# Performance work log

Measured on AMD Instinct MI355X. Metric: run time of the kernel, lower is better.

The kernel has to match this reference:

```python
import jax, jax.numpy as jnp
import numpy as np
from jax import lax

B, T, Tq, S, G, Hd, GW, V = 128, 512, 32, 64, 300, 256, 512, 159
Z = 7 * Hd + 2


def _gru_cell(x, h, Wih, Whh, bih, bhh):
    # torch.nn.GRUCell math (gate order r,z,n)
    gi = x @ Wih.T + bih
    gh = h @ Whh.T + bhh
    i_r, i_z, i_n = jnp.split(gi, 3, axis=-1)
    h_r, h_z, h_n = jnp.split(gh, 3, axis=-1)
    r = jax.nn.sigmoid(i_r + h_r)
    z = jax.nn.sigmoid(i_z + h_z)
    n = jnp.tanh(i_n + r * h_n)
    return (1.0 - z) * n + z * h


def _run_gru(x, Wih, Whh, bih, bhh):
    b = x.shape[0]
    h0 = jnp.zeros((b, Whh.shape[1]), x.dtype)
    def step(h, xt):
        h2 = _gru_cell(xt, h, Wih, Whh, bih, bhh)
        return h2, h2
    _, ys = lax.scan(step, h0, jnp.swapaxes(x, 0, 1))
    return jnp.swapaxes(ys, 0, 1)  # [B,T,H]


def _attention(C, Qv, Mv, zW, gW1, gb1, gW2, gb2):
    # Attention(C, Q, Mt_1) -> Attention_G(c, m=Q, q=Mt_1); vectorized over sentences.
    qb = Qv[:, None, :]   # question, 2nd arg 'm' in Attention_Z
    mb = Mv[:, None, :]   # memory,   3rd arg 'q' in Attention_Z
    cW = jnp.einsum('bsh,kh->bsk', C, zW)  # att_zW(c), no bias
    z = jnp.concatenate([
        C,
        jnp.broadcast_to(qb, C.shape),
        jnp.broadcast_to(mb, C.shape),
        C * mb,                       # c * q  (q = memory)
        C * qb,                       # c * m  (m = question)
        jnp.abs(C - mb),              # |c - q|
        jnp.abs(C - qb),              # |c - m|
        jnp.sum(cW * mb, -1, keepdims=True),  # diag(cW q^T)
        jnp.sum(cW * qb, -1, keepdims=True),  # diag(cW m^T)
    ], axis=-1)  # [B,S,7H+2]
    H1 = jnp.tanh(jnp.einsum('bsz,gz->bsg', z, gW1) + gb1)
    g = jax.nn.sigmoid(jnp.einsum('bsg,og->bso', H1, gW2) + gb2)
    return g[..., 0]  # [B,S]


def setup_inputs() -> dict:
    key = jax.random.key(0)
    ks = jax.random.split(key, 32)
    def p(k, shape):
        return jax.random.normal(k, shape, jnp.float32) * 0.05
    inp = {
        'input': jax.random.normal(ks[0], (B, T, G), jnp.float32),
        'Q': jax.random.normal(ks[1], (B, Tq, G), jnp.float32),
        'EOS_idx': jnp.sort(jax.random.randint(ks[2], (B, S), 0, T), axis=1),
        'q_seq_len': jax.random.randint(ks[3], (B,), 0, Tq),
        'm_depth': 3,
        'a_len': 1,
        # GRU_i
        'Wih_i': p(ks[4], (3 * Hd, G)), 'Whh_i': p(ks[5], (3 * Hd, Hd)),
        'bih_i': p(ks[6], (3 * Hd,)), 'bhh_i': p(ks[7], (3 * Hd,)),
        # GRU_q
        'Wih_q': p(ks[8], (3 * Hd, G)), 'Whh_q': p(ks[9], (3 * Hd, Hd)),
        'bih_q': p(ks[10], (3 * Hd,)), 'bhh_q': p(ks[11], (3 * Hd,)),
        # attention
        'zW': p(ks[12], (Hd, Hd)),
        'gW1': p(ks[13], (GW, Z)), 'gb1': p(ks[14], (GW,)),
        'gW2': p(ks[15], (1, GW)), 'gb2': p(ks[16], (1,)),
        # GRUcell_m
        'Wih_m': p(ks[17], (3 * Hd, Hd)), 'Whh_m': p(ks[18], (3 * Hd, Hd)),
        'bih_m': p(ks[19], (3 * Hd,)), 'bhh_m': p(ks[20], (3 * Hd,)),
        # answer module
        'Wa': p(ks[21], (V, Hd)),
        'Wih_a': p(ks[22], (3 * Hd, Hd + V)), 'Whh_a': p(ks[23], (3 * Hd, Hd)),
        'bih_a': p(ks[24], (3 * Hd,)), 'bhh_a': p(ks[25], (3 * Hd,)),
    }
    return inp


def reference(input, Q, EOS_idx, q_seq_len, m_depth, a_len,
              Wih_i, Whh_i, bih_i, bhh_i,
              Wih_q, Whh_q, bih_q, bhh_q,
              zW, gW1, gb1, gW2, gb2,
              Wih_m, Whh_m, bih_m, bhh_m,
              Wa, Wih_a, Whh_a, bih_a, bhh_a):
    b = input.shape[0]
    # InputModule2: GRU over words, gather hidden states at EOS positions -> facts
    out_i = _run_gru(input, Wih_i, Whh_i, bih_i, bhh_i)          # [B,T,H]
    facts = out_i[jnp.arange(b)[:, None], EOS_idx]               # [B,S,H]
    # QuestionModule2: last valid hidden state of question GRU
    out_q = _run_gru(Q, Wih_q, Whh_q, bih_q, bhh_q)              # [B,Tq,H]
    qidx = jnp.clip(q_seq_len - 1, 0, Q.shape[1] - 1)
    q = out_q[jnp.arange(b), qidx]                               # [B,H]
    # MemoryUpdate (mode='softmax')
    Mt = q
    atts = []
    for _ in range(m_depth):
        att = _attention(facts, q, Mt, zW, gW1, gb1, gW2, gb2)   # [B,S]
        atts.append(att[:, None, :])
        soft = jax.nn.softmax(att, axis=1)
        Htc = jnp.einsum('bsh,bs->bh', facts, soft)              # SoftmaxRep
        Mt = _gru_cell(Htc, Mt, Wih_m, Whh_m, bih_m, bhh_m)
    Attentions = jnp.concatenate(atts, axis=1)                   # [B,depth,S]
    # AnswerModule
    at = Mt
    yt = jax.nn.softmax(at @ Wa.T, axis=1)
    preds = []
    for _ in range(a_len):
        xt = jnp.concatenate([yt, q], axis=1)
        at = _gru_cell(xt, at, Wih_a, Whh_a, bih_a, bhh_a)
        yt = jax.nn.softmax(at @ Wa.T, axis=1)
        preds.append(yt)
    pred = jnp.concatenate(preds, axis=1)                        # [B, a_len*159]
    return pred
```

## Files before the change

### kernel.cpp

```cpp
#include <hip/hip_runtime.h>
#include <hip/hip_bf16.h>

#define B_   128
#define T_   512
#define TQ_  32
#define S_   64
#define G_   300
#define GP_  320
#define HD_  256
#define GW_  512
#define V_   159
#define Z_   1794
#define ZP_  1824
#define H3_  768

using bf16x8 = __attribute__((ext_vector_type(8))) short;
using bf16x4 = __attribute__((ext_vector_type(4))) short;
using f32x4  = __attribute__((ext_vector_type(4))) float;

#define OFF_WIHB_I 0u
#define OFF_WIHB_Q 491520u
#define OFF_GW1B   983040u
#define OFF_FACTS  2850816u
#define OFF_QVEC   11239424u
#define OFF_UQ     11370496u
#define OFF_UM     11501568u
#define OFF_MT     11632640u
#define OFF_HTC    11763712u
#define OFF_YT     12681216u
#define OFF_XT     12762624u
#define OFF_AT2    12975104u
#define OFF_ATT    13106176u
#define OFF_B2I    13139968u
#define OFF_B2Q    13143040u
#define OFF_ABF    16777216u
#define OFF_QBF    16777216u
#define OFF_GIQ    20971520u
#define OFF_Z      29360128u
#define OFF_WMXT   59768832u
#define OFF_WMHT   60555264u
#define OFF_WAXT   61341696u
#define OFF_WAHT   62616576u
#define OFF_GII    67108864u
#define OFF_H1     67108864u

#define WAIT_LGKM0() __builtin_amdgcn_s_waitcnt(0xC07F)

__device__ __forceinline__ unsigned short f2bf(float f) {
    unsigned int u = __float_as_uint(f);
    u += 0x7fffu + ((u >> 16) & 1u);
    return (unsigned short)(u >> 16);
}
__device__ __forceinline__ float bf2f(unsigned short s) {
    return __uint_as_float(((unsigned int)s) << 16);
}
__device__ __forceinline__ float rcpf(float x) { return __builtin_amdgcn_rcpf(x); }
__device__ __forceinline__ float sigm(float x) { return rcpf(1.f + __expf(-x)); }
__device__ __forceinline__ float tanh_fast(float x) {
    float e = __expf(-2.f * fabsf(x));
    float t = (1.f - e) * rcpf(1.f + e);
    return copysignf(t, x);
}

__global__ void conv_pad_kernel(const float* __restrict__ src, unsigned short* __restrict__ dst,
                                int M, int K, int Kp) {
    int i = blockIdx.x * 256 + threadIdx.x;
    if (i >= M * Kp) return;
    int r = i / Kp, c = i - r * Kp;
    dst[i] = (c < K) ? f2bf(src[(size_t)r * K + c]) : (unsigned short)0;
}

#define SEG_A  196608
#define SEG_C  318720
__global__ void prep_kernel(
    const float* __restrict__ Wih_m, float* __restrict__ WmxT,
    const float* __restrict__ Whh_m, float* __restrict__ WmhT,
    const float* __restrict__ Wih_a, float* __restrict__ WaxT,
    const float* __restrict__ Whh_a, float* __restrict__ WahT,
    const float* __restrict__ bih_i, const float* __restrict__ bhh_i, float* __restrict__ b2i,
    const float* __restrict__ bih_q, const float* __restrict__ bhh_q, float* __restrict__ b2q)
{
    int i = blockIdx.x * 256 + threadIdx.x;
    if (i < SEG_A) {
        int r = i / 256, k = i - r * 256;
        WmxT[(size_t)k * 768 + r] = Wih_m[i];
        WmhT[(size_t)k * 768 + r] = Whh_m[i];
        WahT[(size_t)k * 768 + r] = Whh_a[i];
        return;
    }
    i -= SEG_A;
    if (i < SEG_C) {
        int r = i / 415, k = i - r * 415;
        WaxT[(size_t)k * 768 + r] = Wih_a[i];
        return;
    }
    i -= SEG_C;
    if (i < 768) {
        b2i[i] = bih_i[i] + (i < 512 ? bhh_i[i] : 0.f);
        b2q[i] = bih_q[i] + (i < 512 ? bhh_q[i] : 0.f);
    }
}

__global__ __launch_bounds__(256) void gemm_bf16_kernel(
    const unsigned short* __restrict__ A, const unsigned short* __restrict__ W,
    const float* __restrict__ bias, void* __restrict__ Cout,
    int M, int N, int Kp, int act, int out_bf16, int mode, int logT)
{
    __shared__ unsigned short As[64][40];
    __shared__ unsigned short Bs[64][40];
    int tid  = threadIdx.x;
    int wv   = tid >> 6, lane = tid & 63;
    int l15  = lane & 15, q = lane >> 4;
    int n0   = blockIdx.x * 64, m0 = blockIdx.y * 64;
    int r    = tid >> 2, p4 = tid & 3;

    const f32x4 zero4 = {0.f, 0.f, 0.f, 0.f};
    f32x4 acc[4] = {zero4, zero4, zero4, zero4};

    for (int k0 = 0; k0 < Kp; k0 += 32) {
        *(int4*)&As[r][p4 * 8] = *(const int4*)&A[(size_t)(m0 + r) * Kp + k0 + p4 * 8];
        *(int4*)&Bs[r][p4 * 8] = *(const int4*)&W[(size_t)(n0 + r) * Kp + k0 + p4 * 8];
        __syncthreads();
        bf16x8 af = *(const bf16x8*)&As[16 * wv + l15][q * 8];
#pragma unroll
        for (int nt = 0; nt < 4; nt++) {
            bf16x8 bf = *(const bf16x8*)&Bs[16 * nt + l15][q * 8];
            acc[nt] = __builtin_amdgcn_mfma_f32_16x16x32_bf16(af, bf, acc[nt], 0, 0, 0);
        }
        __syncthreads();
    }
    int rb = q * 4;
#pragma unroll
    for (int nt = 0; nt < 4; nt++) {
        int cgate = n0 + 16 * nt + l15;
        float bv = bias ? bias[cgate] : 0.f;
#pragma unroll
        for (int i = 0; i < 4; i++) {
            int row = m0 + 16 * wv + rb + i;
            float v = acc[nt][i] + bv;
            if (act == 1) v = tanh_fast(v);
            if (mode == 1) {
                int Tl = 1 << logT;
                int b = row >> logT, t = row & (Tl - 1);
                int cc = b >> 4, l = b & 15;
                int type = cgate >> 8, h = cgate & 255;
                int wvd = h >> 5, off = h & 31;
                int ttd = off >> 4, qd = (off >> 2) & 3, id = off & 3;
                int tidd = wvd * 64 + qd * 16 + l;
                size_t addr = ((size_t)(cc * Tl + t) * 512 + tidd) * 24 + type * 8 + ttd * 4 + id;
                ((unsigned short*)Cout)[addr] = f2bf(v);
            } else if (out_bf16) {
                ((unsigned short*)Cout)[(size_t)row * N + cgate] = f2bf(v);
            } else {
                ((float*)Cout)[(size_t)row * N + cgate] = v;
            }
        }
    }
}

__global__ __launch_bounds__(512, 2) void gru_rec_kernel(
    const float* __restrict__ Whh0, const float* __restrict__ bhh0,
    const unsigned short* __restrict__ gi0, int T0, const int* __restrict__ g0, int GL0,
    float* __restrict__ dst0,
    const float* __restrict__ Whh1, const float* __restrict__ bhh1,
    const unsigned short* __restrict__ gi1, int T1, const int* __restrict__ g1, int GL1,
    float* __restrict__ dst1)
{
    __shared__ unsigned short hfr[2][8][4][16][8];
    __shared__ int glist[16 * 64];
    __shared__ int gptr[16], gr0s[2][16], gr1s[2][16];
    extern __shared__ unsigned short wnL[];

    int cb  = blockIdx.x;
    int tid = threadIdx.x;
    int wv  = tid >> 6, lane = tid & 63;
    int l15 = lane & 15, q = lane >> 4;

    const float* Whh; const float* bhh; const unsigned short* gi;
    const int* gidx; float* gdst; int T, GL, isq, c;
    if (cb < 8) { Whh = Whh0; bhh = bhh0; gi = gi0; T = T0; gidx = g0; GL = GL0; isq = 0; gdst = dst0; c = cb; }
    else        { Whh = Whh1; bhh = bhh1; gi = gi1; T = T1; gidx = g1; GL = GL1; isq = 1; gdst = dst1; c = cb - 8; }

    bf16x8 wf[5][8];
#pragma unroll
    for (int mt = 0; mt < 5; mt++) {
        int type = (mt < 4) ? (mt >> 1) : 2;
        int tt   = (mt < 4) ? (mt & 1) : 0;
        int g = type * 256 + 32 * wv + 16 * tt + l15;
#pragma unroll
        for (int ks = 0; ks < 8; ks++) {
            float4 w0 = *(const float4*)&Whh[(size_t)g * 256 + ks * 32 + q * 8];
            float4 w1 = *(const float4*)&Whh[(size_t)g * 256 + ks * 32 + q * 8 + 4];
            bf16x8 v;
            v[0] = (short)f2bf(w0.x); v[1] = (short)f2bf(w0.y);
            v[2] = (short)f2bf(w0.z); v[3] = (short)f2bf(w0.w);
            v[4] = (short)f2bf(w1.x); v[5] = (short)f2bf(w1.y);
            v[6] = (short)f2bf(w1.z); v[7] = (short)f2bf(w1.w);
            wf[mt][ks] = v;
        }
    }
    {
        int g = 512 + 32 * wv + 16 + l15;
#pragma unroll
        for (int ks = 0; ks < 8; ks++) {
            float4 w0 = *(const float4*)&Whh[(size_t)g * 256 + ks * 32 + q * 8];
            float4 w1 = *(const float4*)&Whh[(size_t)g * 256 + ks * 32 + q * 8 + 4];
            bf16x8 v;
            v[0] = (short)f2bf(w0.x); v[1] = (short)f2bf(w0.y);
            v[2] = (short)f2bf(w0.z); v[3] = (short)f2bf(w0.w);
            v[4] = (short)f2bf(w1.x); v[5] = (short)f2bf(w1.y);
            v[6] = (short)f2bf(w1.z); v[7] = (short)f2bf(w1.w);
            *(bf16x8*)&wnL[((wv * 8 + ks) * 64 + lane) * 8] = v;
        }
    }
    float bn[2][4];
#pragma unroll
    for (int tt = 0; tt < 2; tt++)
#pragma unroll
        for (int i = 0; i < 4; i++)
            bn[tt][i] = bhh[512 + 32 * wv + 16 * tt + 4 * q + i];

    for (int i2 = tid; i2 < 2048; i2 += 512) ((int*)hfr)[i2] = 0;
    for (int i2 = tid; i2 < 16 * GL; i2 += 512) {
        int b = i2 / GL, s = i2 - b * GL;
        int raw = gidx[(c * 16 + b) * GL + s];
        if (isq) { raw -= 1; if (raw < 0) raw = 0; if (raw > T - 1) raw = T - 1; }
        glist[b * 64 + s] = raw;
    }
    __syncthreads();
    if (tid < 16) {
        int p = 0;
        while (p < GL && glist[tid * 64 + p] == 0) p++;
        gr0s[0][tid] = 0; gr1s[0][tid] = p; gptr[tid] = p;
    }
    __syncthreads();

    float hprev[2][4] = {{0.f, 0.f, 0.f, 0.f}, {0.f, 0.f, 0.f, 0.f}};
    const unsigned short* gib = gi + (size_t)c * T * 12288;
    bf16x8 xa, xb, xc;
    {
        const unsigned short* pv = gib + (size_t)tid * 24;
        xa = *(const bf16x8*)pv;
        xb = *(const bf16x8*)(pv + 8);
        xc = *(const bf16x8*)(pv + 16);
    }

    const f32x4 zero4 = {0.f, 0.f, 0.f, 0.f};
    for (int t = 0; t < T; t++) {
        int cur = t & 1, nxt = cur ^ 1;
        if (tid < 16) {
            int tt1 = t + 1;
            int p = gptr[tid], pp = p;
            while (p < GL && glist[tid * 64 + p] == tt1) p++;
            gr0s[nxt][tid] = pp; gr1s[nxt][tid] = p; gptr[tid] = p;
        }
        f32x4 acc[6];
        acc[0] = zero4; acc[1] = zero4; acc[2] = zero4; acc[3] = zero4;
        {
            f32x4 b4 = {bn[0][0], bn[0][1], bn[0][2], bn[0][3]}; acc[4] = b4;
            f32x4 b5 = {bn[1][0], bn[1][1], bn[1][2], bn[1][3]}; acc[5] = b5;
        }
#pragma unroll
        for (int ks = 0; ks < 8; ks++) {
            bf16x8 hb = *(const bf16x8*)&hfr[cur][ks][q][l15][0];
            acc[0] = __builtin_amdgcn_mfma_f32_16x16x32_bf16(wf[0][ks], hb, acc[0], 0, 0, 0);
            acc[1] = __builtin_amdgcn_mfma_f32_16x16x32_bf16(wf[1][ks], hb, acc[1], 0, 0, 0);
            acc[2] = __builtin_amdgcn_mfma_f32_16x16x32_bf16(wf[2][ks], hb, acc[2], 0, 0, 0);
            acc[3] = __builtin_amdgcn_mfma_f32_16x16x32_bf16(wf[3][ks], hb, acc[3], 0, 0, 0);
            acc[4] = __builtin_amdgcn_mfma_f32_16x16x32_bf16(wf[4][ks], hb, acc[4], 0, 0, 0);
            bf16x8 w5 = *(const bf16x8*)&wnL[((wv * 8 + ks) * 64 + lane) * 8];
            acc[5] = __builtin_amdgcn_mfma_f32_16x16x32_bf16(w5, hb, acc[5], 0, 0, 0);
        }
        float h2a[2][4];
#pragma unroll
        for (int tt = 0; tt < 2; tt++) {
#pragma unroll
            for (int i = 0; i < 4; i++) {
                float r = sigm(bf2f((unsigned short)xa[tt * 4 + i]) + acc[tt][i]);
                float z = sigm(bf2f((unsigned short)xb[tt * 4 + i]) + acc[2 + tt][i]);
                float n = tanh_fast(bf2f((unsigned short)xc[tt * 4 + i]) + r * acc[4 + tt][i]);
                float h2 = (1.f - z) * n + z * hprev[tt][i];
                hprev[tt][i] = h2;
                h2a[tt][i] = h2;
            }
            bf16x4 hb;
#pragma unroll
            for (int i = 0; i < 4; i++) hb[i] = (short)f2bf(h2a[tt][i]);
            int qp = 2 * tt + (q >> 1), jb = 4 * (q & 1);
            *(bf16x4*)&hfr[nxt][wv][qp][l15][jb] = hb;
        }
        {
            int p0 = gr0s[cur][l15], p1 = gr1s[cur][l15];
            for (int s = p0; s < p1; s++) {
                float* dp = &gdst[((size_t)(c * 16 + l15) * GL + s) * 256 + 32 * wv + 4 * q];
                float4 o0 = {h2a[0][0], h2a[0][1], h2a[0][2], h2a[0][3]};
                float4 o1 = {h2a[1][0], h2a[1][1], h2a[1][2], h2a[1][3]};
                *(float4*)dp        = o0;
                *(float4*)(dp + 16) = o1;
            }
        }
        {
            int tn = (t + 1 < T) ? (t + 1) : (T - 1);
            const unsigned short* pv = gib + ((size_t)tn * 512 + tid) * 24;
            xa = *(const bf16x8*)pv;
            xb = *(const bf16x8*)(pv + 8);
            xc = *(const bf16x8*)(pv + 16);
        }
        __builtin_amdgcn_sched_barrier(0);
        WAIT_LGKM0();
        __builtin_amdgcn_s_barrier();
        __builtin_amdgcn_sched_barrier(0);
    }
}

__global__ __launch_bounds__(256) void uvec_kernel(const float* __restrict__ zW,
                                                   const float* __restrict__ v,
                                                   float* __restrict__ u,
                                                   float* __restrict__ vcopy) {
    int b = blockIdx.x, h = threadIdx.x;
    float a = 0.f;
    for (int k = 0; k < 256; k++) a += zW[k * 256 + h] * v[b * 256 + k];
    u[b * 256 + h] = a;
    if (vcopy) vcopy[b * 256 + h] = v[b * 256 + h];
}

__global__ __launch_bounds__(256) void build_z_kernel(
    const float* __restrict__ facts, const float* __restrict__ qv, const float* __restrict__ Mt,
    const float* __restrict__ u_m, const float* __restrict__ u_q, unsigned short* __restrict__ z)
{
    __shared__ float rm[4], rq[4], szm, szq;
    int bs = blockIdx.x;
    int b  = bs >> 6;
    int j  = threadIdx.x;
    float C  = facts[(size_t)bs * 256 + j];
    float m  = Mt[b * 256 + j];
    float qq = qv[b * 256 + j];
    float dm = C * u_m[b * 256 + j];
    float dq = C * u_q[b * 256 + j];
    for (int o = 32; o; o >>= 1) { dm += __shfl_down(dm, o); dq += __shfl_down(dq, o); }
    int wvi = j >> 6;
    if ((j & 63) == 0) { rm[wvi] = dm; rq[wvi] = dq; }
    __syncthreads();
    if (j == 0) { szm = rm[0] + rm[1] + rm[2] + rm[3]; szq = rq[0] + rq[1] + rq[2] + rq[3]; }
    __syncthreads();
    size_t zr = (size_t)bs * ZP_;
    z[zr + j]        = f2bf(C);
    z[zr + 256 + j]  = f2bf(qq);
    z[zr + 512 + j]  = f2bf(m);
    z[zr + 768 + j]  = f2bf(C * m);
    z[zr + 1024 + j] = f2bf(C * qq);
    z[zr + 1280 + j] = f2bf(fabsf(C - m));
    z[zr + 1536 + j] = f2bf(fabsf(C - qq));
    if (j == 0) { z[zr + 1792] = f2bf(szm); z[zr + 1793] = f2bf(szq); }
    if (j < ZP_ - Z_) z[zr + Z_ + j] = 0;
}

__global__ __launch_bounds__(256) void g_reduce_kernel(const float* __restrict__ H1,
                                                       const float* __restrict__ gW2,
                                                       const float* __restrict__ gb2,
                                                       float* __restrict__ att) {
    __shared__ float r[4];
    int row = blockIdx.x, tid = threadIdx.x;
    float a = H1[(size_t)row * 512 + tid] * gW2[tid]
            + H1[(size_t)row * 512 + 256 + tid] * gW2[256 + tid];
    for (int o = 32; o; o >>= 1) a += __shfl_down(a, o);
    if ((tid & 63) == 0) r[tid >> 6] = a;
    __syncthreads();
    if (tid == 0) att[row] = sigm(r[0] + r[1] + r[2] + r[3] + gb2[0]);
}

__global__ __launch_bounds__(256) void soft_htc_kernel(const float* __restrict__ att,
                                                       const float* __restrict__ facts,
                                                       float* __restrict__ Htc) {
    __shared__ float p[64];
    int b = blockIdx.x, tid = threadIdx.x;
    if (tid < 64) p[tid] = att[b * 64 + tid];
    __syncthreads();
    if (tid == 0) {
        float mx = -1e30f;
        for (int s = 0; s < 64; s++) mx = fmaxf(mx, p[s]);
        float sm = 0.f;
        for (int s = 0; s < 64; s++) { float e = __expf(p[s] - mx); p[s] = e; sm += e; }
        float inv = rcpf(sm);
        for (int s = 0; s < 64; s++) p[s] *= inv;
    }
    __syncthreads();
    float a = 0.f;
    for (int s = 0; s < 64; s++) a += facts[((size_t)b * 64 + s) * 256 + tid] * p[s];
    Htc[b * 256 + tid] = a;
}

__global__ __launch_bounds__(256) void cell_kernel(
    const float* __restrict__ x, int Kx, const float* __restrict__ WxT, const float* __restrict__ bx,
    const float* __restrict__ h, const float* __restrict__ WhT, const float* __restrict__ bh,
    float* __restrict__ hnew)
{
    __shared__ float xs[416], hs[256];
    int b = blockIdx.x, j = threadIdx.x;
    for (int i = j; i < Kx; i += 256) xs[i] = x[(size_t)b * Kx + i];
    hs[j] = h[b * 256 + j];
    __syncthreads();
    float ar = bx[j], az = bx[256 + j], an = bx[512 + j];
    for (int k = 0; k < Kx; k++) {
        float xv = xs[k];
        const float* wr = &WxT[(size_t)k * 768];
        ar += xv * wr[j]; az += xv * wr[256 + j]; an += xv * wr[512 + j];
    }
    float hr = bh[j], hz = bh[256 + j], hn = bh[512 + j];
    for (int k = 0; k < 256; k++) {
        float hv = hs[k];
        const float* wr = &WhT[(size_t)k * 768];
        hr += hv * wr[j]; hz += hv * wr[256 + j]; hn += hv * wr[512 + j];
    }
    float r = sigm(ar + hr);
    float z = sigm(az + hz);
    float n = tanh_fast(an + r * hn);
    hnew[b * 256 + j] = (1.f - z) * n + z * hs[j];
}

__global__ __launch_bounds__(256) void matvec_softmax_kernel(const float* __restrict__ src,
                                                             const float* __restrict__ Wa,
                                                             float* __restrict__ dst) {
    __shared__ float sc[V_];
    int b = blockIdx.x, tid = threadIdx.x;
    if (tid < V_) {
        float a = 0.f;
        for (int k = 0; k < 256; k++) a += src[b * 256 + k] * Wa[tid * 256 + k];
        sc[tid] = a;
    }
    __syncthreads();
    if (tid == 0) {
        float mx = -1e30f;
        for (int v = 0; v < V_; v++) mx = fmaxf(mx, sc[v]);
        float sm = 0.f;
        for (int v = 0; v < V_; v++) { float e = __expf(sc[v] - mx); sc[v] = e; sm += e; }
        float inv = rcpf(sm);
        for (int v = 0; v < V_; v++) sc[v] *= inv;
    }
    __syncthreads();
    if (tid < V_) dst[b * V_ + tid] = sc[tid];
}

__global__ void concat_xt_kernel(const float* __restrict__ yt, const float* __restrict__ qv,
                                 float* __restrict__ xt) {
    int i = blockIdx.x * 256 + threadIdx.x;
    if (i >= 128 * 415) return;
    int b = i / 415, j = i - b * 415;
    xt[i] = (j < V_) ? yt[b * V_ + j] : qv[b * 256 + (j - V_)];
}

extern "C" void kernel_launch(void* const* d_in, const int* in_sizes, int n_in,
                              void* d_out, int out_size, void* d_ws, size_t ws_size,
                              hipStream_t stream) {
    (void)in_sizes; (void)n_in; (void)out_size; (void)ws_size;
    const float* input = (const float*)d_in[0];
    const float* Qin   = (const float*)d_in[1];
    const int*   EOS   = (const int*)d_in[2];
    const int*   qsl   = (const int*)d_in[3];
    const float* Wih_i = (const float*)d_in[6];
    const float* Whh_i = (const float*)d_in[7];
    const float* bih_i = (const float*)d_in[8];
    const float* bhh_i = (const float*)d_in[9];
    const float* Wih_q = (const float*)d_in[10];
    const float* Whh_q = (const float*)d_in[11];
    const float* bih_q = (const float*)d_in[12];
    const float* bhh_q = (const float*)d_in[13];
    const float* zW    = (const float*)d_in[14];
    const float* gW1   = (const float*)d_in[15];
    const float* gb1   = (const float*)d_in[16];
    const float* gW2   = (const float*)d_in[17];
    const float* gb2   = (const float*)d_in[18];
    const float* Wih_m = (const float*)d_in[19];
    const float* Whh_m = (const float*)d_in[20];
    const float* bih_m = (const float*)d_in[21];
    const float* bhh_m = (const float*)d_in[22];
    const float* Wa    = (const float*)d_in[23];
    const float* Wih_a = (const float*)d_in[24];
    const float* Whh_a = (const float*)d_in[25];
    const float* bih_a = (const float*)d_in[26];
    const float* bhh_a = (const float*)d_in[27];

    char* ws = (char*)d_ws;
    unsigned short* Wihb_i = (unsigned short*)(ws + OFF_WIHB_I);
    unsigned short* Wihb_q = (unsigned short*)(ws + OFF_WIHB_Q);
    unsigned short* gW1b   = (unsigned short*)(ws + OFF_GW1B);
    float* facts = (float*)(ws + OFF_FACTS);
    float* qvec  = (float*)(ws + OFF_QVEC);
    float* u_q   = (float*)(ws + OFF_UQ);
    float* u_m   = (float*)(ws + OFF_UM);
    float* Mt    = (float*)(ws + OFF_MT);
    float* Htc   = (float*)(ws + OFF_HTC);
    float* yt    = (float*)(ws + OFF_YT);
    float* xt    = (float*)(ws + OFF_XT);
    float* at2   = (float*)(ws + OFF_AT2);
    float* att   = (float*)(ws + OFF_ATT);
    float* b2i   = (float*)(ws + OFF_B2I);
    float* b2q   = (float*)(ws + OFF_B2Q);
    float* WmxT  = (float*)(ws + OFF_WMXT);
    float* WmhT  = (float*)(ws + OFF_WMHT);
    float* WaxT  = (float*)(ws + OFF_WAXT);
    float* WahT  = (float*)(ws + OFF_WAHT);
    unsigned short* Abf  = (unsigned short*)(ws + OFF_ABF);
    unsigned short* Qbf  = (unsigned short*)(ws + OFF_QBF);
    unsigned short* gi_q = (unsigned short*)(ws + OFF_GIQ);
    unsigned short* zbf  = (unsigned short*)(ws + OFF_Z);
    unsigned short* gi_i = (unsigned short*)(ws + OFF_GII);
    float* H1 = (float*)(ws + OFF_H1);

    hipFuncSetAttribute((const void*)gru_rec_kernel,
                        hipFuncAttributeMaxDynamicSharedMemorySize, 65536);

    conv_pad_kernel<<<(65536 * GP_ + 255) / 256, 256, 0, stream>>>(input, Abf, 65536, G_, GP_);
    conv_pad_kernel<<<(H3_ * GP_ + 255) / 256, 256, 0, stream>>>(Wih_i, Wihb_i, H3_, G_, GP_);
    conv_pad_kernel<<<(H3_ * GP_ + 255) / 256, 256, 0, stream>>>(Wih_q, Wihb_q, H3_, G_, GP_);
    conv_pad_kernel<<<(GW_ * ZP_ + 255) / 256, 256, 0, stream>>>(gW1, gW1b, GW_, Z_, ZP_);
    prep_kernel<<<(SEG_A + SEG_C + 768 + 255) / 256, 256, 0, stream>>>(
        Wih_m, WmxT, Whh_m, WmhT, Wih_a, WaxT, Whh_a, WahT,
        bih_i, bhh_i, b2i, bih_q, bhh_q, b2q);
    gemm_bf16_kernel<<<dim3(12, 1024), 256, 0, stream>>>(Abf, Wihb_i, b2i, gi_i, 65536, H3_, GP_, 0, 1, 1, 9);
    conv_pad_kernel<<<(4096 * GP_ + 255) / 256, 256, 0, stream>>>(Qin, Qbf, 4096, G_, GP_);
    gemm_bf16_kernel<<<dim3(12, 64), 256, 0, stream>>>(Qbf, Wihb_q, b2q, gi_q, 4096, H3_, GP_, 0, 1, 1, 5);
    gru_rec_kernel<<<16, 512, 65536, stream>>>(Whh_i, bhh_i, gi_i, T_, EOS, S_, facts,
                                               Whh_q, bhh_q, gi_q, TQ_, qsl, 1, qvec);
    uvec_kernel<<<128, 256, 0, stream>>>(zW, qvec, u_q, Mt);
    for (int ep = 0; ep < 3; ep++) {
        uvec_kernel<<<128, 256, 0, stream>>>(zW, Mt, u_m, nullptr);
        build_z_kernel<<<8192, 256, 0, stream>>>(facts, qvec, Mt, u_m, u_q, zbf);
        gemm_bf16_kernel<<<dim3(8, 128), 256, 0, stream>>>(zbf, gW1b, gb1, H1, 8192, GW_, ZP_, 1, 0, 0, 0);
        g_reduce_kernel<<<8192, 256, 0, stream>>>(H1, gW2, gb2, att);
        soft_htc_kernel<<<128, 256, 0, stream>>>(att, facts, Htc);
        cell_kernel<<<128, 256, 0, stream>>>(Htc, 256, WmxT, bih_m, Mt, WmhT, bhh_m, Mt);
    }
    matvec_softmax_kernel<<<128, 256, 0, stream>>>(Mt, Wa, yt);
    concat_xt_kernel<<<(128 * 415 + 255) / 256, 256, 0, stream>>>(yt, qvec, xt);
    cell_kernel<<<128, 256, 0, stream>>>(xt, 415, WaxT, bih_a, Mt, WahT, bhh_a, at2);
    matvec_softmax_kernel<<<128, 256, 0, stream>>>(at2, Wa, (float*)d_out);
}
```

Measured before the change: 1.802 ms.

## Fuse episode tail, answer and prep kernels; prefetch GRU inputs two steps ahead

```diff
diff --git a/kernel.cpp b/kernel.cpp
--- a/kernel.cpp
+++ b/kernel.cpp
@@ -26,15 +26,10 @@
 #define OFF_UQ     11370496u
 #define OFF_UM     11501568u
 #define OFF_MT     11632640u
-#define OFF_HTC    11763712u
-#define OFF_YT     12681216u
-#define OFF_XT     12762624u
-#define OFF_AT2    12975104u
-#define OFF_ATT    13106176u
 #define OFF_B2I    13139968u
 #define OFF_B2Q    13143040u
+#define OFF_QBF    13500416u
 #define OFF_ABF    16777216u
-#define OFF_QBF    16777216u
 #define OFF_GIQ    20971520u
 #define OFF_Z      29360128u
 #define OFF_WMXT   59768832u
@@ -70,34 +65,62 @@
     dst[i] = (c < K) ? f2bf(src[(size_t)r * K + c]) : (unsigned short)0;
 }
 
-#define SEG_A  196608
-#define SEG_C  318720
+#define S1_ 196608
+#define S2_ 318720
+#define S3_ 768
+#define S4_ 245760
+#define S5_ 933888
+#define S6_ 1310720
+#define PREP_TOT (S1_ + S2_ + S3_ + S4_ + S5_ + S6_)
 __global__ void prep_kernel(
     const float* __restrict__ Wih_m, float* __restrict__ WmxT,
     const float* __restrict__ Whh_m, float* __restrict__ WmhT,
     const float* __restrict__ Wih_a, float* __restrict__ WaxT,
     const float* __restrict__ Whh_a, float* __restrict__ WahT,
     const float* __restrict__ bih_i, const float* __restrict__ bhh_i, float* __restrict__ b2i,
-    const float* __restrict__ bih_q, const float* __restrict__ bhh_q, float* __restrict__ b2q)
+    const float* __restrict__ bih_q, const float* __restrict__ bhh_q, float* __restrict__ b2q,
+    const float* __restrict__ Wih_i, unsigned short* __restrict__ Wihb_i,
+    const float* __restrict__ Wih_q, unsigned short* __restrict__ Wihb_q,
+    const float* __restrict__ gW1,   unsigned short* __restrict__ gW1b,
+    const float* __restrict__ Qin,   unsigned short* __restrict__ Qbf)
 {
     int i = blockIdx.x * 256 + threadIdx.x;
-    if (i < SEG_A) {
+    if (i < S1_) {
         int r = i / 256, k = i - r * 256;
         WmxT[(size_t)k * 768 + r] = Wih_m[i];
         WmhT[(size_t)k * 768 + r] = Whh_m[i];
         WahT[(size_t)k * 768 + r] = Whh_a[i];
         return;
     }
-    i -= SEG_A;
-    if (i < SEG_C) {
+    i -= S1_;
+    if (i < S2_) {
         int r = i / 415, k = i - r * 415;
         WaxT[(size_t)k * 768 + r] = Wih_a[i];
         return;
     }
-    i -= SEG_C;
-    if (i < 768) {
+    i -= S2_;
+    if (i < S3_) {
         b2i[i] = bih_i[i] + (i < 512 ? bhh_i[i] : 0.f);
         b2q[i] = bih_q[i] + (i < 512 ? bhh_q[i] : 0.f);
+        return;
+    }
+    i -= S3_;
+    if (i < S4_) {
+        int r = i / GP_, c = i - r * GP_;
+        Wihb_i[i] = (c < G_) ? f2bf(Wih_i[(size_t)r * G_ + c]) : (unsigned short)0;
+        Wihb_q[i] = (c < G_) ? f2bf(Wih_q[(size_t)r * G_ + c]) : (unsigned short)0;
+        return;
+    }
+    i -= S4_;
+    if (i < S5_) {
+        int r = i / ZP_, c = i - r * ZP_;
+        gW1b[i] = (c < Z_) ? f2bf(gW1[(size_t)r * Z_ + c]) : (unsigned short)0;
+        return;
+    }
+    i -= S5_;
+    if (i < S6_) {
+        int r = i / GP_, c = i - r * GP_;
+        Qbf[i] = (c < G_) ? f2bf(Qin[(size_t)r * G_ + c]) : (unsigned short)0;
     }
 }
 
@@ -237,16 +260,17 @@
 
     float hprev[2][4] = {{0.f, 0.f, 0.f, 0.f}, {0.f, 0.f, 0.f, 0.f}};
     const unsigned short* gib = gi + (size_t)c * T * 12288;
-    bf16x8 xa, xb, xc;
+    const f32x4 zero4 = {0.f, 0.f, 0.f, 0.f};
+
+    bf16x8 xa0, xb0, xc0, xa1, xb1, xc1;
     {
         const unsigned short* pv = gib + (size_t)tid * 24;
-        xa = *(const bf16x8*)pv;
-        xb = *(const bf16x8*)(pv + 8);
-        xc = *(const bf16x8*)(pv + 16);
-    }
-
-    const f32x4 zero4 = {0.f, 0.f, 0.f, 0.f};
-    for (int t = 0; t < T; t++) {
+        xa0 = *(const bf16x8*)pv; xb0 = *(const bf16x8*)(pv + 8); xc0 = *(const bf16x8*)(pv + 16);
+        const unsigned short* pw = gib + ((size_t)512 + tid) * 24;
+        xa1 = *(const bf16x8*)pw; xb1 = *(const bf16x8*)(pw + 8); xc1 = *(const bf16x8*)(pw + 16);
+    }
+
+    auto do_step = [&](int t, bf16x8& Xa, bf16x8& Xb, bf16x8& Xc) {
         int cur = t & 1, nxt = cur ^ 1;
         if (tid < 16) {
             int tt1 = t + 1;
@@ -276,9 +300,9 @@
         for (int tt = 0; tt < 2; tt++) {
 #pragma unroll
             for (int i = 0; i < 4; i++) {
-                float r = sigm(bf2f((unsigned short)xa[tt * 4 + i]) + acc[tt][i]);
-                float z = sigm(bf2f((unsigned short)xb[tt * 4 + i]) + acc[2 + tt][i]);
-                float n = tanh_fast(bf2f((unsigned short)xc[tt * 4 + i]) + r * acc[4 + tt][i]);
+                float r = sigm(bf2f((unsigned short)Xa[tt * 4 + i]) + acc[tt][i]);
+                float z = sigm(bf2f((unsigned short)Xb[tt * 4 + i]) + acc[2 + tt][i]);
+                float n = tanh_fast(bf2f((unsigned short)Xc[tt * 4 + i]) + r * acc[4 + tt][i]);
                 float h2 = (1.f - z) * n + z * hprev[tt][i];
                 hprev[tt][i] = h2;
                 h2a[tt][i] = h2;
@@ -300,28 +324,35 @@
             }
         }
         {
-            int tn = (t + 1 < T) ? (t + 1) : (T - 1);
+            int tn = (t + 2 < T) ? (t + 2) : (T - 1);
             const unsigned short* pv = gib + ((size_t)tn * 512 + tid) * 24;
-            xa = *(const bf16x8*)pv;
-            xb = *(const bf16x8*)(pv + 8);
-            xc = *(const bf16x8*)(pv + 16);
+            Xa = *(const bf16x8*)pv;
+            Xb = *(const bf16x8*)(pv + 8);
+            Xc = *(const bf16x8*)(pv + 16);
         }
         __builtin_amdgcn_sched_barrier(0);
         WAIT_LGKM0();
         __builtin_amdgcn_s_barrier();
         __builtin_amdgcn_sched_barrier(0);
+    };
+
+    for (int t = 0; t < T; t += 2) {
+        do_step(t,     xa0, xb0, xc0);
+        do_step(t + 1, xa1, xb1, xc1);
     }
 }
 
 __global__ __launch_bounds__(256) void uvec_kernel(const float* __restrict__ zW,
                                                    const float* __restrict__ v,
-                                                   float* __restrict__ u,
-                                                   float* __restrict__ vcopy) {
+                                                   float* __restrict__ u_q,
+                                                   float* __restrict__ u_m,
+                                                   float* __restrict__ Mt) {
     int b = blockIdx.x, h = threadIdx.x;
     float a = 0.f;
     for (int k = 0; k < 256; k++) a += zW[k * 256 + h] * v[b * 256 + k];
-    u[b * 256 + h] = a;
-    if (vcopy) vcopy[b * 256 + h] = v[b * 256 + h];
+    u_q[b * 256 + h] = a;
+    u_m[b * 256 + h] = a;
+    Mt[b * 256 + h]  = v[b * 256 + h];
 }
 
 __global__ __launch_bounds__(256) void build_z_kernel(
@@ -355,77 +386,91 @@
     if (j < ZP_ - Z_) z[zr + Z_ + j] = 0;
 }
 
-__global__ __launch_bounds__(256) void g_reduce_kernel(const float* __restrict__ H1,
-                                                       const float* __restrict__ gW2,
-                                                       const float* __restrict__ gb2,
-                                                       float* __restrict__ att) {
-    __shared__ float r[4];
-    int row = blockIdx.x, tid = threadIdx.x;
-    float a = H1[(size_t)row * 512 + tid] * gW2[tid]
-            + H1[(size_t)row * 512 + 256 + tid] * gW2[256 + tid];
-    for (int o = 32; o; o >>= 1) a += __shfl_down(a, o);
-    if ((tid & 63) == 0) r[tid >> 6] = a;
-    __syncthreads();
-    if (tid == 0) att[row] = sigm(r[0] + r[1] + r[2] + r[3] + gb2[0]);
-}
-
-__global__ __launch_bounds__(256) void soft_htc_kernel(const float* __restrict__ att,
-                                                       const float* __restrict__ facts,
-                                                       float* __restrict__ Htc) {
-    __shared__ float p[64];
+__global__ __launch_bounds__(256) void episode_tail_kernel(
+    const float* __restrict__ H1, const float* __restrict__ gW2, const float* __restrict__ gb2,
+    const float* __restrict__ facts,
+    const float* __restrict__ WmxT, const float* __restrict__ bxm,
+    const float* __restrict__ WmhT, const float* __restrict__ bhm,
+    const float* __restrict__ zW,
+    float* __restrict__ Mt, float* __restrict__ u_m)
+{
+    __shared__ float red[64][4];
+    __shared__ float p64[64];
+    __shared__ float xs[256];
+    __shared__ float hs[256];
+    __shared__ float hs2[256];
     int b = blockIdx.x, tid = threadIdx.x;
-    if (tid < 64) p[tid] = att[b * 64 + tid];
-    __syncthreads();
-    if (tid == 0) {
-        float mx = -1e30f;
-        for (int s = 0; s < 64; s++) mx = fmaxf(mx, p[s]);
-        float sm = 0.f;
-        for (int s = 0; s < 64; s++) { float e = __expf(p[s] - mx); p[s] = e; sm += e; }
-        float inv = rcpf(sm);
-        for (int s = 0; s < 64; s++) p[s] *= inv;
-    }
-    __syncthreads();
-    float a = 0.f;
-    for (int s = 0; s < 64; s++) a += facts[((size_t)b * 64 + s) * 256 + tid] * p[s];
-    Htc[b * 256 + tid] = a;
-}
-
-__global__ __launch_bounds__(256) void cell_kernel(
-    const float* __restrict__ x, int Kx, const float* __restrict__ WxT, const float* __restrict__ bx,
-    const float* __restrict__ h, const float* __restrict__ WhT, const float* __restrict__ bh,
-    float* __restrict__ hnew)
+    {
+        int s = tid >> 2, part = tid & 3;
+        const float* h1r = H1 + ((size_t)(b * 64 + s)) * 512 + part * 128;
+        const float* w2  = gW2 + part * 128;
+        float a = 0.f;
+        for (int k = 0; k < 128; k++) a += h1r[k] * w2[k];
+        red[s][part] = a;
+    }
+    hs[tid] = Mt[b * 256 + tid];
+    __syncthreads();
+    if (tid < 64) {
+        float att = sigm(red[tid][0] + red[tid][1] + red[tid][2] + red[tid][3] + gb2[0]);
+        float mx = att;
+        for (int o = 32; o; o >>= 1) mx = fmaxf(mx, __shfl_xor(mx, o));
+        float e = __expf(att - mx);
+        float sm = e;
+        for (int o = 32; o; o >>= 1) sm += __shfl_xor(sm, o);
+        p64[tid] = e * rcpf(sm);
+    }
+    __syncthreads();
+    {
+        float a = 0.f;
+        for (int s = 0; s < 64; s++) a += facts[((size_t)b * 64 + s) * 256 + tid] * p64[s];
+        xs[tid] = a;
+    }
+    __syncthreads();
+    {
+        int j = tid;
+        float ar = bxm[j], az = bxm[256 + j], an = bxm[512 + j];
+        for (int k = 0; k < 256; k++) {
+            float xv = xs[k];
+            const float* wr = &WmxT[(size_t)k * 768];
+            ar += xv * wr[j]; az += xv * wr[256 + j]; an += xv * wr[512 + j];
+        }
+        float hr = bhm[j], hz = bhm[256 + j], hn = bhm[512 + j];
+        for (int k = 0; k < 256; k++) {
+            float hv = hs[k];
+            const float* wr = &WmhT[(size_t)k * 768];
+            hr += hv * wr[j]; hz += hv * wr[256 + j]; hn += hv * wr[512 + j];
+        }
+        float r = sigm(ar + hr);
+        float z = sigm(az + hz);
+        float n = tanh_fast(an + r * hn);
+        float h2 = (1.f - z) * n + z * hs[j];
+        Mt[b * 256 + j] = h2;
+        hs2[j] = h2;
+    }
+    __syncthreads();
+    {
+        float a = 0.f;
+        for (int k = 0; k < 256; k++) a += zW[k * 256 + tid] * hs2[k];
+        u_m[b * 256 + tid] = a;
+    }
+}
+
+__global__ __launch_bounds__(256) void answer_kernel(
+    const float* __restrict__ Mt, const float* __restrict__ Wa, const float* __restrict__ qv,
+    const float* __restrict__ WaxT, const float* __restrict__ bxa,
+    const float* __restrict__ WahT, const float* __restrict__ bha,
+    float* __restrict__ out)
 {
-    __shared__ float xs[416], hs[256];
-    int b = blockIdx.x, j = threadIdx.x;
-    for (int i = j; i < Kx; i += 256) xs[i] = x[(size_t)b * Kx + i];
-    hs[j] = h[b * 256 + j];
-    __syncthreads();
-    float ar = bx[j], az = bx[256 + j], an = bx[512 + j];
-    for (int k = 0; k < Kx; k++) {
-        float xv = xs[k];
-        const float* wr = &WxT[(size_t)k * 768];
-        ar += xv * wr[j]; az += xv * wr[256 + j]; an += xv * wr[512 + j];
-    }
-    float hr = bh[j], hz = bh[256 + j], hn = bh[512 + j];
-    for (int k = 0; k < 256; k++) {
-        float hv = hs[k];
-        const float* wr = &WhT[(size_t)k * 768];
-        hr += hv * wr[j]; hz += hv * wr[256 + j]; hn += hv * wr[512 + j];
-    }
-    float r = sigm(ar + hr);
-    float z = sigm(az + hz);
-    float n = tanh_fast(an + r * hn);
-    hnew[b * 256 + j] = (1.f - z) * n + z * hs[j];
-}
-
-__global__ __launch_bounds__(256) void matvec_softmax_kernel(const float* __restrict__ src,
-                                                             const float* __restrict__ Wa,
-                                                             float* __restrict__ dst) {
     __shared__ float sc[V_];
+    __shared__ float xs[416];
+    __shared__ float hs[256], hs2[256];
     int b = blockIdx.x, tid = threadIdx.x;
+    hs[tid] = Mt[b * 256 + tid];
+    xs[V_ + tid] = qv[b * 256 + tid];
+    __syncthreads();
     if (tid < V_) {
         float a = 0.f;
-        for (int k = 0; k < 256; k++) a += src[b * 256 + k] * Wa[tid * 256 + k];
+        for (int k = 0; k < 256; k++) a += hs[k] * Wa[(size_t)tid * 256 + k];
         sc[tid] = a;
     }
     __syncthreads();
@@ -438,15 +483,44 @@
         for (int v = 0; v < V_; v++) sc[v] *= inv;
     }
     __syncthreads();
-    if (tid < V_) dst[b * V_ + tid] = sc[tid];
-}
-
-__global__ void concat_xt_kernel(const float* __restrict__ yt, const float* __restrict__ qv,
-                                 float* __restrict__ xt) {
-    int i = blockIdx.x * 256 + threadIdx.x;
-    if (i >= 128 * 415) return;
-    int b = i / 415, j = i - b * 415;
-    xt[i] = (j < V_) ? yt[b * V_ + j] : qv[b * 256 + (j - V_)];
+    if (tid < V_) xs[tid] = sc[tid];
+    __syncthreads();
+    {
+        int j = tid;
+        float ar = bxa[j], az = bxa[256 + j], an = bxa[512 + j];
+        for (int k = 0; k < 415; k++) {
+            float xv = xs[k];
+            const float* wr = &WaxT[(size_t)k * 768];
+            ar += xv * wr[j]; az += xv * wr[256 + j]; an += xv * wr[512 + j];
+        }
+        float hr = bha[j], hz = bha[256 + j], hn = bha[512 + j];
+        for (int k = 0; k < 256; k++) {
+            float hv = hs[k];
+            const float* wr = &WahT[(size_t)k * 768];
+            hr += hv * wr[j]; hz += hv * wr[256 + j]; hn += hv * wr[512 + j];
+        }
+        float r = sigm(ar + hr);
+        float z = sigm(az + hz);
+        float n = tanh_fast(an + r * hn);
+        hs2[j] = (1.f - z) * n + z * hs[j];
+    }
+    __syncthreads();
+    if (tid < V_) {
+        float a = 0.f;
+        for (int k = 0; k < 256; k++) a += hs2[k] * Wa[(size_t)tid * 256 + k];
+        sc[tid] = a;
+    }
+    __syncthreads();
+    if (tid == 0) {
+        float mx = -1e30f;
+        for (int v = 0; v < V_; v++) mx = fmaxf(mx, sc[v]);
+        float sm = 0.f;
+        for (int v = 0; v < V_; v++) { float e = __expf(sc[v] - mx); sc[v] = e; sm += e; }
+        float inv = rcpf(sm);
+        for (int v = 0; v < V_; v++) sc[v] *= inv;
+    }
+    __syncthreads();
+    if (tid < V_) out[b * V_ + tid] = sc[tid];
 }
 
 extern "C" void kernel_launch(void* const* d_in, const int* in_sizes, int n_in,
@@ -489,11 +563,6 @@
     float* u_q   = (float*)(ws + OFF_UQ);
     float* u_m   = (float*)(ws + OFF_UM);
     float* Mt    = (float*)(ws + OFF_MT);
-    float* Htc   = (float*)(ws + OFF_HTC);
-    float* yt    = (float*)(ws + OFF_YT);
-    float* xt    = (float*)(ws + OFF_XT);
-    float* at2   = (float*)(ws + OFF_AT2);
-    float* att   = (float*)(ws + OFF_ATT);
     float* b2i   = (float*)(ws + OFF_B2I);
     float* b2q   = (float*)(ws + OFF_B2Q);
     float* WmxT  = (float*)(ws + OFF_WMXT);
@@ -511,28 +580,20 @@
                         hipFuncAttributeMaxDynamicSharedMemorySize, 65536);
 
     conv_pad_kernel<<<(65536 * GP_ + 255) / 256, 256, 0, stream>>>(input, Abf, 65536, G_, GP_);
-    conv_pad_kernel<<<(H3_ * GP_ + 255) / 256, 256, 0, stream>>>(Wih_i, Wihb_i, H3_, G_, GP_);
-    conv_pad_kernel<<<(H3_ * GP_ + 255) / 256, 256, 0, stream>>>(Wih_q, Wihb_q, H3_, G_, GP_);
-    conv_pad_kernel<<<(GW_ * ZP_ + 255) / 256, 256, 0, stream>>>(gW1, gW1b, GW_, Z_, ZP_);
-    prep_kernel<<<(SEG_A + SEG_C + 768 + 255) / 256, 256, 0, stream>>>(
+    prep_kernel<<<(PREP_TOT + 255) / 256, 256, 0, stream>>>(
         Wih_m, WmxT, Whh_m, WmhT, Wih_a, WaxT, Whh_a, WahT,
-        bih_i, bhh_i, b2i, bih_q, bhh_q, b2q);
+        bih_i, bhh_i, b2i, bih_q, bhh_q, b2q,
+        Wih_i, Wihb_i, Wih_q, Wihb_q, gW1, gW1b, Qin, Qbf);
     gemm_bf16_kernel<<<dim3(12, 1024), 256, 0, stream>>>(Abf, Wihb_i, b2i, gi_i, 65536, H3_, GP_, 0, 1, 1, 9);
-    conv_pad_kernel<<<(4096 * GP_ + 255) / 256, 256, 0, stream>>>(Qin, Qbf, 4096, G_, GP_);
     gemm_bf16_kernel<<<dim3(12, 64), 256, 0, stream>>>(Qbf, Wihb_q, b2q, gi_q, 4096, H3_, GP_, 0, 1, 1, 5);
     gru_rec_kernel<<<16, 512, 65536, stream>>>(Whh_i, bhh_i, gi_i, T_, EOS, S_, facts,
                                                Whh_q, bhh_q, gi_q, TQ_, qsl, 1, qvec);
-    uvec_kernel<<<128, 256, 0, stream>>>(zW, qvec, u_q, Mt);
+    uvec_kernel<<<128, 256, 0, stream>>>(zW, qvec, u_q, u_m, Mt);
     for (int ep = 0; ep < 3; ep++) {
-        uvec_kernel<<<128, 256, 0, stream>>>(zW, Mt, u_m, nullptr);
         build_z_kernel<<<8192, 256, 0, stream>>>(facts, qvec, Mt, u_m, u_q, zbf);
         gemm_bf16_kernel<<<dim3(8, 128), 256, 0, stream>>>(zbf, gW1b, gb1, H1, 8192, GW_, ZP_, 1, 0, 0, 0);
-        g_reduce_kernel<<<8192, 256, 0, stream>>>(H1, gW2, gb2, att);
-        soft_htc_kernel<<<128, 256, 0, stream>>>(att, facts, Htc);
-        cell_kernel<<<128, 256, 0, stream>>>(Htc, 256, WmxT, bih_m, Mt, WmhT, bhh_m, Mt);
-    }
-    matvec_softmax_kernel<<<128, 256, 0, stream>>>(Mt, Wa, yt);
-    concat_xt_kernel<<<(128 * 415 + 255) / 256, 256, 0, stream>>>(yt, qvec, xt);
-    cell_kernel<<<128, 256, 0, stream>>>(xt, 415, WaxT, bih_a, Mt, WahT, bhh_a, at2);
-    matvec_softmax_kernel<<<128, 256, 0, stream>>>(at2, Wa, (float*)d_out);
-}
+        episode_tail_kernel<<<128, 256, 0, stream>>>(H1, gW2, gb2, facts,
+                                                     WmxT, bih_m, WmhT, bhh_m, zW, Mt, u_m);
+    }
+    answer_kernel<<<128, 256, 0, stream>>>(Mt, Wa, qvec, WaxT, bih_a, WahT, bhh_a, (float*)d_out);
+}
```

After: 1.935 ms. 1.07x slower.
